# Optimization experiments

Hardware: AMD Instinct MI355X
Metric: run time of the kernel (lower is better)

## Reference

```python
import jax, jax.numpy as jnp
import numpy as np

INF = 1000000000000.0
V, H, E, B, T, S, NUM_OOV = 32000, 512, 300, 32, 32, 400, 50


def setup_inputs() -> dict:
    key = jax.random.key(0)
    ks = jax.random.split(key, 20)
    sc = 0.02
    inp = {
        'trg_seq_embedded': jax.random.normal(ks[0], (B, T, E), jnp.float32),
        'ext_src_seq': jax.random.randint(ks[1], (B, S), 0, V + NUM_OOV, jnp.int32),
        'init_states': jax.random.normal(ks[2], (1, B, H), jnp.float32),
        'encoder_outputs': jax.random.normal(ks[3], (B, S, H), jnp.float32),
        'encoder_mask': jax.random.randint(ks[4], (B, S), 0, 2, jnp.int32),
        # parameters (PyTorch Linear convention: y = x @ W.T + b)
        'W_enc': sc * jax.random.normal(ks[5], (H, H), jnp.float32),
        'b_enc': jnp.zeros((H,), jnp.float32),
        'W_red': sc * jax.random.normal(ks[6], (E, E + H), jnp.float32),
        'b_red': jnp.zeros((E,), jnp.float32),
        'W_ih': sc * jax.random.normal(ks[7], (4 * H, E), jnp.float32),
        'W_hh': sc * jax.random.normal(ks[8], (4 * H, H), jnp.float32),
        'b_ih': jnp.zeros((4 * H,), jnp.float32),
        'b_hh': jnp.zeros((4 * H,), jnp.float32),
        'W_cat': sc * jax.random.normal(ks[9], (H, 2 * H), jnp.float32),
        'b_cat': jnp.zeros((H,), jnp.float32),
        'W_log': sc * jax.random.normal(ks[10], (V, H), jnp.float32),
        'b_log': jnp.zeros((V,), jnp.float32),
    }
    return inp


def decoder_forward(trg_seq_embedded, init_states, encoder_outputs,
                    W_enc, b_enc, W_red, b_red, W_ih, W_hh, b_ih, b_hh,
                    W_cat, b_cat, W_log, b_log, ext_src_seq, encoder_mask):
    batch, max_len, _ = trg_seq_embedded.shape
    src_len = encoder_outputs.shape[1]
    hidden = encoder_outputs.shape[-1]
    memories = encoder_outputs @ W_enc.T + b_enc            # [B,S,H]
    mask0 = (encoder_mask == 0)                              # [B,S]
    bidx = jnp.arange(batch)[:, None]                        # [B,1]

    h0 = init_states[0]
    c0 = init_states[0]
    ctx0 = jnp.zeros((batch, hidden), trg_seq_embedded.dtype)
    cov0 = jnp.zeros((batch, src_len), trg_seq_embedded.dtype)

    def step(carry, emb_t):
        h, c, prev_ctx, cov = carry
        x = jnp.concatenate([emb_t, prev_ctx], axis=-1) @ W_red.T + b_red
        gates = x @ W_ih.T + b_ih + h @ W_hh.T + b_hh
        i, f, g, o = jnp.split(gates, 4, axis=-1)
        c_new = jax.nn.sigmoid(f) * c + jax.nn.sigmoid(i) * jnp.tanh(g)
        h_new = jax.nn.sigmoid(o) * jnp.tanh(c_new)
        energy = jnp.einsum('bh,bsh->bs', h_new, memories)
        energy = jnp.where(mask0, -INF, energy)
        attn = jax.nn.softmax(energy, axis=-1)
        ctx = jnp.einsum('bs,bsh->bh', attn, memories)
        logit_in = jnp.tanh(jnp.concatenate([h_new, ctx], axis=-1) @ W_cat.T + b_cat)
        logit = logit_in @ W_log.T + b_log                   # [B,V]
        ext = jnp.concatenate([logit, jnp.zeros((batch, NUM_OOV), logit.dtype)], axis=1)
        out = jnp.full_like(ext, -INF).at[bidx, ext_src_seq].max(energy)
        out = jnp.where(out == -INF, 0.0, out)
        logit_ext = ext + out
        logit_ext = jnp.where(logit_ext == 0.0, -INF, logit_ext)
        return (h_new, c_new, ctx, cov + attn), (logit_ext, attn, cov, energy)

    _, (logits, attns, covs, energies) = jax.lax.scan(
        step, (h0, c0, ctx0, cov0), jnp.swapaxes(trg_seq_embedded, 0, 1))
    return logits, attns, covs, energies


def reference(trg_seq_embedded, ext_src_seq, init_states, encoder_outputs, encoder_mask,
              W_enc, b_enc, W_red, b_red, W_ih, W_hh, b_ih, b_hh,
              W_cat, b_cat, W_log, b_log):
    return decoder_forward(trg_seq_embedded, init_states, encoder_outputs,
                           W_enc, b_enc, W_red, b_red, W_ih, W_hh, b_ih, b_hh,
                           W_cat, b_cat, W_log, b_log, ext_src_seq, encoder_mask)
```

## Files before the change

kernel.cpp:

```cpp
#include <hip/hip_runtime.h>
#include <hip/hip_bf16.h>

#define INF_F 1000000000000.0f

typedef __attribute__((ext_vector_type(8))) short bfrag8;
typedef __attribute__((ext_vector_type(4))) float facc4;
typedef __attribute__((ext_vector_type(4))) short short4v;

__device__ __forceinline__ float sigf(float x){ return 1.0f/(1.0f + expf(-x)); }
__device__ __forceinline__ short f2bf(float f){
  __hip_bfloat16 h = __float2bfloat16(f);
  return *reinterpret_cast<short*>(&h);
}
__device__ __forceinline__ float bf2f(short s){
  unsigned u = ((unsigned)(unsigned short)s) << 16;
  return *reinterpret_cast<float*>(&u);
}

#define OFF_LOG 0ull
#define OFF_A   32819200ull
#define OFF_C   33228800ull
#define OFF_E   33638400ull

__global__ __launch_bounds__(256) void k_init(const float* __restrict__ init_s,
    float* __restrict__ hbuf, float* __restrict__ c0, float* __restrict__ ctxb,
    float* __restrict__ cov) {
  int i = blockIdx.x*256 + threadIdx.x;
  if (i < 32*512) { float v = init_s[i]; hbuf[i]=v; c0[i]=v; ctxb[i]=0.0f; }
  if (i < 32*400) cov[i] = 0.0f;
}

__global__ __launch_bounds__(256) void k_bcombo(const float* __restrict__ W_ih,
    const float* __restrict__ b_red, const float* __restrict__ b_ih,
    const float* __restrict__ b_hh, float* __restrict__ bcomb) {
  int j = blockIdx.x*256 + threadIdx.x;
  if (j >= 2048) return;
  float acc = b_ih[j] + b_hh[j];
  for (int m=0;m<300;m++) acc += W_ih[j*300+m]*b_red[m];
  bcomb[j] = acc;
}

__global__ __launch_bounds__(256) void k_wcombo(const float* __restrict__ W_ih,
    const float* __restrict__ W_red, float* __restrict__ Wct) {
  __shared__ float As[16][68];
  __shared__ float Bs[16][68];
  int tid = threadIdx.x;
  int m0 = blockIdx.y*64, n0 = blockIdx.x*64;
  int rl = tid>>2, kq = (tid&3)*4;
  int kl = tid>>4, c4 = (tid&15)*4;
  int tx = tid&15, ty = tid>>4;
  float acc[4][4]={};
  for (int kk=0;kk<300;kk+=16){
    #pragma unroll
    for (int q=0;q<4;q++){
      int kg = kk+kq+q;
      As[kq+q][rl] = (kg<300) ? W_ih[(size_t)(m0+rl)*300 + kg] : 0.0f;
    }
    #pragma unroll
    for (int q=0;q<4;q++){
      int c = n0 + c4 + q;
      Bs[kl][c4+q] = (kk+kl<300 && c<812) ? W_red[(size_t)(kk+kl)*812 + c] : 0.0f;
    }
    __syncthreads();
    #pragma unroll
    for (int k=0;k<16;k++){
      const float* ap=&As[k][ty*4]; const float* bp=&Bs[k][tx*4];
      #pragma unroll
      for (int i=0;i<4;i++)
        #pragma unroll
        for (int j=0;j<4;j++) acc[i][j] += ap[i]*bp[j];
    }
    __syncthreads();
  }
  #pragma unroll
  for (int i=0;i<4;i++)
    #pragma unroll
    for (int j=0;j<4;j++){
      int row = m0+ty*4+i, col = n0+tx*4+j;
      if (col<812) Wct[(size_t)row*812 + col] = acc[i][j];
    }
}

__global__ __launch_bounds__(256) void k_gemb(const float* __restrict__ trg,
    const float* __restrict__ Wct, const float* __restrict__ bcomb,
    float* __restrict__ Gemb) {
  __shared__ float As[16][68];
  __shared__ float Bs[16][68];
  int tid = threadIdx.x;
  int m0 = blockIdx.y*64, n0 = blockIdx.x*64;
  int rl = tid>>2, kq = (tid&3)*4;
  int tx = tid&15, ty = tid>>4;
  float acc[4][4]={};
  int r = m0 + rl;
  const float* arow = trg + (size_t)(r&31)*9600 + (size_t)(r>>5)*300;
  for (int kk=0;kk<300;kk+=16){
    #pragma unroll
    for (int q=0;q<4;q++){
      int kg = kk+kq+q;
      As[kq+q][rl] = (kg<300) ? arow[kg] : 0.0f;
      Bs[kq+q][rl] = (kg<300) ? Wct[(size_t)(n0+rl)*812 + kg] : 0.0f;
    }
    __syncthreads();
    #pragma unroll
    for (int k=0;k<16;k++){
      const float* ap=&As[k][ty*4]; const float* bp=&Bs[k][tx*4];
      #pragma unroll
      for (int i=0;i<4;i++)
        #pragma unroll
        for (int j=0;j<4;j++) acc[i][j] += ap[i]*bp[j];
    }
    __syncthreads();
  }
  #pragma unroll
  for (int i=0;i<4;i++)
    #pragma unroll
    for (int j=0;j<4;j++){
      int rr = m0+ty*4+i, col = n0+tx*4+j;
      Gemb[(size_t)rr*2048 + col] = acc[i][j] + bcomb[col];
    }
}

__global__ __launch_bounds__(256) void k_wgpack(const float* __restrict__ Wct,
    const float* __restrict__ W_hh, float* __restrict__ Wg) {
  int idx = blockIdx.x*256 + threadIdx.x;
  if (idx >= 1024*2048) return;
  int k = idx >> 11, j = idx & 2047;
  Wg[idx] = (k < 512) ? Wct[(size_t)j*812 + 300 + k] : W_hh[(size_t)j*512 + (k-512)];
}

__global__ __launch_bounds__(256) void k_convsplit(const float* __restrict__ enc,
    const float* __restrict__ W_enc, short* __restrict__ ehi, short* __restrict__ elo,
    short* __restrict__ whi, short* __restrict__ wlo) {
  int i4 = blockIdx.x*256 + threadIdx.x;
  const float* src; short* dhi; short* dlo; size_t off;
  if (i4 < 1638400) { src = enc;   dhi = ehi; dlo = elo; off = (size_t)i4*4; }
  else { int j4 = i4 - 1638400; if (j4 >= 65536) return;
         src = W_enc; dhi = whi; dlo = wlo; off = (size_t)j4*4; }
  float4 v = *(const float4*)(src + off);
  float f[4] = {v.x, v.y, v.z, v.w};
  short4v h, l;
  #pragma unroll
  for (int q=0;q<4;q++){
    short hb = f2bf(f[q]);
    float r = f[q] - bf2f(hb);
    h[q] = hb; l[q] = f2bf(r);
  }
  *(short4v*)(dhi + off) = h;
  *(short4v*)(dlo + off) = l;
}

__device__ __forceinline__ int lds_off(int row, int slot) {
  return (row<<6) + (((slot ^ ((row>>1)&3))&3)<<4);
}

__global__ __launch_bounds__(256) void k_memories(const short* __restrict__ Ahg,
    const short* __restrict__ Alg, const short* __restrict__ Bhg,
    const short* __restrict__ Blg, const float* __restrict__ bias,
    float* __restrict__ mem) {
  __shared__ short Ah[4096];
  __shared__ short Al[4096];
  __shared__ short Bh[4096];
  __shared__ short Bl[4096];
  int tid = threadIdx.x;
  int m0 = blockIdx.x*128, n0 = blockIdx.y*128;
  int w = tid>>6, lane = tid&63;
  int wr = w>>1, wc = w&1;
  int lr = lane&15, kg2 = lane>>4;

  int srow = tid>>1;
  int ss   = (tid&1)*2;
  const short* gah = Ahg + (size_t)(m0+srow)*512 + ss*8;
  const short* gal = Alg + (size_t)(m0+srow)*512 + ss*8;
  const short* gbh = Bhg + (size_t)(n0+srow)*512 + ss*8;
  const short* gbl = Blg + (size_t)(n0+srow)*512 + ss*8;
  int wo0 = lds_off(srow, ss), wo1 = lds_off(srow, ss+1);

  int raoff[4], rboff[4];
  #pragma unroll
  for (int q=0;q<4;q++){
    raoff[q] = lds_off(wr*64 + q*16 + lr, kg2);
    rboff[q] = lds_off(wc*64 + q*16 + lr, kg2);
  }

  facc4 acc[4][4] = {};
  bfrag8 rah0 = *(const bfrag8*)(gah);
  bfrag8 rah1 = *(const bfrag8*)(gah+8);
  bfrag8 ral0 = *(const bfrag8*)(gal);
  bfrag8 ral1 = *(const bfrag8*)(gal+8);
  bfrag8 rbh0 = *(const bfrag8*)(gbh);
  bfrag8 rbh1 = *(const bfrag8*)(gbh+8);
  bfrag8 rbl0 = *(const bfrag8*)(gbl);
  bfrag8 rbl1 = *(const bfrag8*)(gbl+8);

  for (int i=0;i<16;i++){
    __syncthreads();
    *(bfrag8*)((char*)Ah + wo0) = rah0;
    *(bfrag8*)((char*)Ah + wo1) = rah1;
    *(bfrag8*)((char*)Al + wo0) = ral0;
    *(bfrag8*)((char*)Al + wo1) = ral1;
    *(bfrag8*)((char*)Bh + wo0) = rbh0;
    *(bfrag8*)((char*)Bh + wo1) = rbh1;
    *(bfrag8*)((char*)Bl + wo0) = rbl0;
    *(bfrag8*)((char*)Bl + wo1) = rbl1;
    __syncthreads();
    if (i<15){
      gah += 32; gal += 32; gbh += 32; gbl += 32;
      rah0 = *(const bfrag8*)(gah);
      rah1 = *(const bfrag8*)(gah+8);
      ral0 = *(const bfrag8*)(gal);
      ral1 = *(const bfrag8*)(gal+8);
      rbh0 = *(const bfrag8*)(gbh);
      rbh1 = *(const bfrag8*)(gbh+8);
      rbl0 = *(const bfrag8*)(gbl);
      rbl1 = *(const bfrag8*)(gbl+8);
    }
    bfrag8 afh[4], afl[4], bfh[4], bfl[4];
    #pragma unroll
    for (int q=0;q<4;q++){
      afh[q] = *(const bfrag8*)((char*)Ah + raoff[q]);
      afl[q] = *(const bfrag8*)((char*)Al + raoff[q]);
      bfh[q] = *(const bfrag8*)((char*)Bh + rboff[q]);
      bfl[q] = *(const bfrag8*)((char*)Bl + rboff[q]);
    }
    #pragma unroll
    for (int mi=0;mi<4;mi++)
      #pragma unroll
      for (int ni=0;ni<4;ni++){
        acc[mi][ni] = __builtin_amdgcn_mfma_f32_16x16x32_bf16(afl[mi], bfh[ni], acc[mi][ni], 0,0,0);
        acc[mi][ni] = __builtin_amdgcn_mfma_f32_16x16x32_bf16(afh[mi], bfl[ni], acc[mi][ni], 0,0,0);
        acc[mi][ni] = __builtin_amdgcn_mfma_f32_16x16x32_bf16(afh[mi], bfh[ni], acc[mi][ni], 0,0,0);
      }
  }

  #pragma unroll
  for (int mi=0;mi<4;mi++){
    int row = m0 + wr*64 + mi*16 + kg2*4;
    #pragma unroll
    for (int ni=0;ni<4;ni++){
      int col = n0 + wc*64 + ni*16 + lr;
      float bl = bias[col];
      #pragma unroll
      for (int q=0;q<4;q++)
        mem[(size_t)(row+q)*512 + col] = acc[mi][ni][q] + bl;
    }
  }
}

__global__ __launch_bounds__(256) void k_wlogconv(const float* __restrict__ W_log,
    __hip_bfloat16* __restrict__ wlb, const float* __restrict__ W_cat,
    short* __restrict__ wcatb) {
  int i4 = blockIdx.x*256 + threadIdx.x;
  if (i4 < 4096000) {
    const float4 v = *(const float4*)(W_log + (size_t)i4*4);
    size_t o = (size_t)i4*4;
    wlb[o+0] = __float2bfloat16(v.x); wlb[o+1] = __float2bfloat16(v.y);
    wlb[o+2] = __float2bfloat16(v.z); wlb[o+3] = __float2bfloat16(v.w);
  } else {
    int j4 = i4 - 4096000;
    if (j4 >= 131072) return;
    const float4 v = *(const float4*)(W_cat + (size_t)j4*4);
    short4v s;
    s[0]=f2bf(v.x); s[1]=f2bf(v.y); s[2]=f2bf(v.z); s[3]=f2bf(v.w);
    *(short4v*)(wcatb + (size_t)j4*4) = s;
  }
}

__global__ __launch_bounds__(256) void k_catconv(const float* __restrict__ hall,
    const float* __restrict__ ctxa, short* __restrict__ licat) {
  int i4 = blockIdx.x*256 + threadIdx.x;
  if (i4 >= 262144) return;
  int row = i4 >> 8, colq = (i4 & 255) * 4;
  const float* src = (colq < 512) ? (hall + (size_t)row*512 + colq)
                                  : (ctxa + (size_t)row*512 + colq - 512);
  float4 v = *(const float4*)src;
  short4v s;
  s[0]=f2bf(v.x); s[1]=f2bf(v.y); s[2]=f2bf(v.z); s[3]=f2bf(v.w);
  *(short4v*)(licat + (size_t)i4*4) = s;
}

__global__ __launch_bounds__(256) void k_gates(const float* __restrict__ ctxb,
    const float* __restrict__ hbuf, const float* __restrict__ Wg,
    float* __restrict__ partials) {
  __shared__ float yh_s[64][32];
  int ks = blockIdx.x;
  int rc = blockIdx.y;
  int tid = threadIdx.x;
  const float* side = (ks < 8) ? ctxb : hbuf;
  int kbase = (ks & 7) * 64;
  {
    int b_l = tid >> 3, kq0 = (tid & 7) * 8;
    const float* src = side + (size_t)b_l*512 + kbase + kq0;
    float4 v0 = *(const float4*)(src);
    float4 v1 = *(const float4*)(src + 4);
    yh_s[kq0+0][b_l]=v0.x; yh_s[kq0+1][b_l]=v0.y;
    yh_s[kq0+2][b_l]=v0.z; yh_s[kq0+3][b_l]=v0.w;
    yh_s[kq0+4][b_l]=v1.x; yh_s[kq0+5][b_l]=v1.y;
    yh_s[kq0+6][b_l]=v1.z; yh_s[kq0+7][b_l]=v1.w;
  }
  __syncthreads();
  int tr = tid & 31, bg = tid >> 5;
  int row0 = rc*128 + tr*4;
  float acc[4][4] = {};
  const float* wp = Wg + (size_t)(ks*64)*2048 + row0;
  #pragma unroll 8
  for (int k=0;k<64;k++){
    float4 w = *(const float4*)(wp + (size_t)k*2048);
    float4 y = *(const float4*)&yh_s[k][bg*4];
    acc[0][0]+=w.x*y.x; acc[0][1]+=w.x*y.y; acc[0][2]+=w.x*y.z; acc[0][3]+=w.x*y.w;
    acc[1][0]+=w.y*y.x; acc[1][1]+=w.y*y.y; acc[1][2]+=w.y*y.z; acc[1][3]+=w.y*y.w;
    acc[2][0]+=w.z*y.x; acc[2][1]+=w.z*y.y; acc[2][2]+=w.z*y.z; acc[2][3]+=w.z*y.w;
    acc[3][0]+=w.w*y.x; acc[3][1]+=w.w*y.y; acc[3][2]+=w.w*y.z; acc[3][3]+=w.w*y.w;
  }
  #pragma unroll
  for (int j=0;j<4;j++){
    float4 o; o.x=acc[0][j]; o.y=acc[1][j]; o.z=acc[2][j]; o.w=acc[3][j];
    *(float4*)(partials + (size_t)(ks*32 + bg*4 + j)*2048 + row0) = o;
  }
}

__global__ __launch_bounds__(256) void k_lstm_energy(const float* __restrict__ part,
    const float* __restrict__ Gemb,
    const float* __restrict__ c_in, float* __restrict__ c_out,
    float* __restrict__ hbuf, float* __restrict__ hall,
    const float* __restrict__ mem, const int* __restrict__ emask,
    float* __restrict__ out, int t) {
  __shared__ float hl[512];
  int blk = blockIdx.x, tid = threadIdx.x;
  int b = blk & 31, sc = blk >> 5;
  int r = t*32 + b;
  int lane = tid & 63, w = tid >> 6;
  const float* gp = Gemb + (size_t)r*2048;
  #pragma unroll
  for (int jj=0; jj<2; jj++){
    int j = tid + jj*256;
    float g[4];
    #pragma unroll
    for (int gi=0; gi<4; gi++){
      int row = gi*512 + j;
      float v = gp[row];
      #pragma unroll
      for (int ks=0; ks<16; ks++)
        v += part[(size_t)(ks*32+b)*2048 + row];
      g[gi] = v;
    }
    float cp = c_in[b*512+j];
    float cn = sigf(g[1])*cp + sigf(g[0])*tanhf(g[2]);
    float hn = sigf(g[3])*tanhf(cn);
    hl[j] = hn;
    if (sc==0){
      c_out[b*512+j]=cn; hbuf[b*512+j]=hn; hall[(size_t)r*512+j]=hn;
    }
  }
  __syncthreads();
  float4 h0 = *(const float4*)&hl[lane*8];
  float4 h1 = *(const float4*)&hl[lane*8+4];
  const float* mb = mem + (size_t)b*204800;
  const int* em = emask + b*400;
  for (int i=0;i<13;i++){
    int s_l = i*4 + w;
    if (s_l < 50){
      int s = sc*50 + s_l;
      const float4* mp = (const float4*)(mb + (size_t)s*512 + lane*8);
      float4 m0 = mp[0], m1 = mp[1];
      float acc = h0.x*m0.x + h0.y*m0.y + h0.z*m0.z + h0.w*m0.w
                + h1.x*m1.x + h1.y*m1.y + h1.z*m1.z + h1.w*m1.w;
      #pragma unroll
      for (int off=32; off; off>>=1) acc += __shfl_xor(acc, off);
      if (lane==0){
        out[OFF_E + (size_t)r*400 + s] = (em[s]==0) ? -INF_F : acc;
      }
    }
  }
}

__global__ __launch_bounds__(256) void k_ctx(float* __restrict__ out,
    const float* __restrict__ mem, float* __restrict__ ctxb, float* __restrict__ ctxa,
    float* __restrict__ cov, int t) {
  __shared__ float ps[400];
  __shared__ float red[8];
  __shared__ float tmp[256];
  int blk = blockIdx.x, tid = threadIdx.x;
  int b = blk & 31, hc = blk >> 5;
  int r = t*32 + b;
  int lane = tid & 63, w = tid >> 6;
  float e0 = out[OFF_E + (size_t)r*400 + tid];
  float e1 = (tid < 144) ? out[OFF_E + (size_t)r*400 + tid + 256] : -3.4e38f;
  float lm = fmaxf(e0, e1);
  #pragma unroll
  for (int off=32; off; off>>=1) lm = fmaxf(lm, __shfl_xor(lm, off));
  if (lane==0) red[w] = lm;
  __syncthreads();
  float m = fmaxf(fmaxf(red[0],red[1]), fmaxf(red[2],red[3]));
  float pv0 = expf(e0 - m);
  float pv1 = (tid < 144) ? expf(e1 - m) : 0.0f;
  float sv = pv0 + pv1;
  #pragma unroll
  for (int off=32; off; off>>=1) sv += __shfl_xor(sv, off);
  if (lane==0) red[4+w] = sv;
  __syncthreads();
  float inv = 1.0f/(red[4]+red[5]+red[6]+red[7]);
  ps[tid] = pv0*inv;
  if (tid < 144) ps[tid+256] = pv1*inv;
  __syncthreads();
  int hloc = tid & 63, sh = tid >> 6;
  int h = hc*64 + hloc;
  float acc = 0.0f;
  {
    const float* mqs = mem + (size_t)b*204800 + h + (size_t)sh*100*512;
    const float* pss = &ps[sh*100];
    #pragma unroll 10
    for (int s=0;s<100;s++) acc += pss[s]*mqs[(size_t)s*512];
  }
  tmp[sh*64 + hloc] = acc;
  __syncthreads();
  if (sh==0){
    float v = acc + tmp[64+hloc] + tmp[128+hloc] + tmp[192+hloc];
    ctxb[b*512+h] = v;
    ctxa[(size_t)r*512+h] = v;
  }
  if (hc==0){
    for (int s=tid; s<400; s+=256){
      float a = ps[s];
      out[OFF_A + (size_t)r*400 + s] = a;
      float cv = cov[b*400+s];
      out[OFF_C + (size_t)r*400 + s] = cv;
      cov[b*400+s] = cv + a;
    }
  }
}

__global__ __launch_bounds__(256) void k_logitin(const short* __restrict__ Ab,
    const short* __restrict__ Wb, const float* __restrict__ b_cat,
    __hip_bfloat16* __restrict__ lib) {
  __shared__ short As[4096];
  __shared__ short Bs[4096];
  int tid = threadIdx.x;
  int m0 = blockIdx.x*128, n0 = blockIdx.y*128;
  int w = tid>>6, lane = tid&63;
  int wr = w>>1, wc = w&1;
  int lr = lane&15, kg2 = lane>>4;

  int srow = tid>>1;
  int ss   = (tid&1)*2;
  const short* ga = Ab + (size_t)(m0+srow)*1024 + ss*8;
  const short* gw = Wb + (size_t)(n0+srow)*1024 + ss*8;
  int wo0 = lds_off(srow, ss), wo1 = lds_off(srow, ss+1);

  int raoff[4], rboff[4];
  #pragma unroll
  for (int q=0;q<4;q++){
    raoff[q] = lds_off(wr*64 + q*16 + lr, kg2);
    rboff[q] = lds_off(wc*64 + q*16 + lr, kg2);
  }

  facc4 acc[4][4] = {};
  bfrag8 ra0 = *(const bfrag8*)(ga);
  bfrag8 ra1 = *(const bfrag8*)(ga+8);
  bfrag8 rb0 = *(const bfrag8*)(gw);
  bfrag8 rb1 = *(const bfrag8*)(gw+8);

  for (int i=0;i<32;i++){
    __syncthreads();
    *(bfrag8*)((char*)As + wo0) = ra0;
    *(bfrag8*)((char*)As + wo1) = ra1;
    *(bfrag8*)((char*)Bs + wo0) = rb0;
    *(bfrag8*)((char*)Bs + wo1) = rb1;
    __syncthreads();
    if (i<31){
      ga += 32; gw += 32;
      ra0 = *(const bfrag8*)(ga);
      ra1 = *(const bfrag8*)(ga+8);
      rb0 = *(const bfrag8*)(gw);
      rb1 = *(const bfrag8*)(gw+8);
    }
    bfrag8 af[4], bf[4];
    #pragma unroll
    for (int q=0;q<4;q++){
      af[q] = *(const bfrag8*)((char*)As + raoff[q]);
      bf[q] = *(const bfrag8*)((char*)Bs + rboff[q]);
    }
    #pragma unroll
    for (int mi=0;mi<4;mi++)
      #pragma unroll
      for (int ni=0;ni<4;ni++)
        acc[mi][ni] = __builtin_amdgcn_mfma_f32_16x16x32_bf16(af[mi], bf[ni], acc[mi][ni], 0,0,0);
  }

  #pragma unroll
  for (int mi=0;mi<4;mi++){
    int row = m0 + wr*64 + mi*16 + kg2*4;
    #pragma unroll
    for (int ni=0;ni<4;ni++){
      int col = n0 + wc*64 + ni*16 + lr;
      float bc = b_cat[col];
      #pragma unroll
      for (int q=0;q<4;q++){
        float v = tanhf(acc[mi][ni][q] + bc);
        lib[(size_t)(row+q)*512 + col] = __float2bfloat16(v);
      }
    }
  }
}

__global__ __launch_bounds__(256) void k_logits(const __hip_bfloat16* __restrict__ Ab,
    const __hip_bfloat16* __restrict__ Wb, const float* __restrict__ b_log,
    float* __restrict__ out) {
  __shared__ short As[4096];
  __shared__ short Bs[4096];
  int m = blockIdx.y & 7;
  int yy = blockIdx.x + 8*(blockIdx.y >> 3);
  if (yy >= 250) return;
  int tid = threadIdx.x;
  int m0 = m*128, n0 = yy*128;
  int w = tid>>6, lane = tid&63;
  int wr = w>>1, wc = w&1;
  int lr = lane&15, kg2 = lane>>4;
  const short* A = (const short*)Ab;
  const short* W = (const short*)Wb;

  int srow = tid>>1;
  int ss   = (tid&1)*2;
  const short* ga = A + (size_t)(m0+srow)*512 + ss*8;
  const short* gw = W + (size_t)(n0+srow)*512 + ss*8;
  int wo0 = lds_off(srow, ss), wo1 = lds_off(srow, ss+1);

  int raoff[4], rboff[4];
  #pragma unroll
  for (int q=0;q<4;q++){
    raoff[q] = lds_off(wr*64 + q*16 + lr, kg2);
    rboff[q] = lds_off(wc*64 + q*16 + lr, kg2);
  }

  facc4 acc[4][4] = {};
  bfrag8 ra0 = *(const bfrag8*)(ga);
  bfrag8 ra1 = *(const bfrag8*)(ga+8);
  bfrag8 rb0 = *(const bfrag8*)(gw);
  bfrag8 rb1 = *(const bfrag8*)(gw+8);

  for (int i=0;i<16;i++){
    __syncthreads();
    *(bfrag8*)((char*)As + wo0) = ra0;
    *(bfrag8*)((char*)As + wo1) = ra1;
    *(bfrag8*)((char*)Bs + wo0) = rb0;
    *(bfrag8*)((char*)Bs + wo1) = rb1;
    __syncthreads();
    if (i<15){
      ga += 32; gw += 32;
      ra0 = *(const bfrag8*)(ga);
      ra1 = *(const bfrag8*)(ga+8);
      rb0 = *(const bfrag8*)(gw);
      rb1 = *(const bfrag8*)(gw+8);
    }
    bfrag8 af[4], bf[4];
    #pragma unroll
    for (int q=0;q<4;q++){
      af[q] = *(const bfrag8*)((char*)As + raoff[q]);
      bf[q] = *(const bfrag8*)((char*)Bs + rboff[q]);
    }
    #pragma unroll
    for (int mi=0;mi<4;mi++)
      #pragma unroll
      for (int ni=0;ni<4;ni++)
        acc[mi][ni] = __builtin_amdgcn_mfma_f32_16x16x32_bf16(af[mi], bf[ni], acc[mi][ni], 0,0,0);
  }

  #pragma unroll
  for (int mi=0;mi<4;mi++){
    int row = m0 + wr*64 + mi*16 + kg2*4;
    #pragma unroll
    for (int ni=0;ni<4;ni++){
      int col = n0 + wc*64 + ni*16 + lr;
      float bl = b_log[col];
      #pragma unroll
      for (int q=0;q<4;q++){
        float v = acc[mi][ni][q] + bl;
        out[(size_t)(row+q)*32050 + col] = (v == 0.0f) ? -INF_F : v;
      }
    }
  }
}

__global__ __launch_bounds__(512) void k_scatter(const int* __restrict__ ext_src,
    float* __restrict__ out) {
  __shared__ int tok[400];
  __shared__ float ev[400];
  int rr = blockIdx.x;
  int b = rr & 31;
  int tid = threadIdx.x;
  if (tid >= 400 && tid < 450)
    out[(size_t)rr*32050 + 32000 + (tid-400)] = -INF_F;
  if (tid < 400){
    tok[tid] = ext_src[b*400+tid];
    ev[tid]  = out[OFF_E + (size_t)rr*400 + tid];
  }
  __syncthreads();
  if (tid < 400){
    int tk = tok[tid];
    float m = -3.4e38f;
    bool pre = false;
    #pragma unroll 1
    for (int s2=0; s2<400; s2+=8){
      #pragma unroll
      for (int q=0;q<8;q++){
        int tk2 = tok[s2+q];
        float e2 = ev[s2+q];
        bool eq = (tk2==tk);
        m = fmaxf(m, eq ? e2 : -3.4e38f);
        pre = pre || (eq && (s2+q) < tid);
      }
    }
    if (!pre && m != -INF_F){
      size_t idx = (size_t)rr*32050 + tk;
      float wv = out[idx];
      float extv = (wv == -INF_F) ? 0.0f : wv;
      float nv = extv + m;
      out[idx] = (nv == 0.0f) ? -INF_F : nv;
    }
  }
}

extern "C" void kernel_launch(void* const* d_in, const int* in_sizes, int n_in,
                              void* d_out, int out_size, void* d_ws, size_t ws_size,
                              hipStream_t stream) {
  const float* trg   = (const float*)d_in[0];
  const int*   ext   = (const int*)  d_in[1];
  const float* inits = (const float*)d_in[2];
  const float* enc   = (const float*)d_in[3];
  const int*   emask = (const int*)  d_in[4];
  const float* W_enc = (const float*)d_in[5];
  const float* b_enc = (const float*)d_in[6];
  const float* W_red = (const float*)d_in[7];
  const float* b_red = (const float*)d_in[8];
  const float* W_ih  = (const float*)d_in[9];
  const float* W_hh  = (const float*)d_in[10];
  const float* b_ih  = (const float*)d_in[11];
  const float* b_hh  = (const float*)d_in[12];
  const float* W_cat = (const float*)d_in[13];
  const float* b_cat = (const float*)d_in[14];
  const float* W_log = (const float*)d_in[15];
  const float* b_log = (const float*)d_in[16];
  float* out = (float*)d_out;
  float* ws  = (float*)d_ws;

  float* mem   = ws + 0ull;
  float* Wg    = ws + 6553600ull;
  float* Wct   = ws + 8650752ull;
  float* Gemb  = ws + 10313728ull;
  float* bcomb = ws + 12410880ull;
  float* hbuf  = ws + 12412928ull;
  float* c0    = ws + 12429312ull;
  float* c1    = ws + 12445696ull;
  float* ctxb  = ws + 12462080ull;
  float* hall  = ws + 12478464ull;
  float* ctxa  = ws + 13002752ull;
  float* cov   = ws + 13527040ull;
  float* part  = ws + 13539840ull;
  __hip_bfloat16* lib = (__hip_bfloat16*)(ws + 14590464ull);
  short* licat = (short*)(ws + 8650752ull);
  short* wcatb = (short*)(ws + 9175040ull);
  __hip_bfloat16* wlb = (__hip_bfloat16*)(ws + 15245824ull);
  short* ehi = (short*)(ws + 15245824ull);
  short* elo = ehi + 6553600;
  short* whi = ehi + 13107200;
  short* wlo = ehi + 13369344;

  k_init<<<64,256,0,stream>>>(inits, hbuf, c0, ctxb, cov);
  k_bcombo<<<8,256,0,stream>>>(W_ih, b_red, b_ih, b_hh, bcomb);
  k_wcombo<<<dim3(13,32),256,0,stream>>>(W_ih, W_red, Wct);
  k_gemb<<<dim3(32,16),256,0,stream>>>(trg, Wct, bcomb, Gemb);
  k_wgpack<<<8192,256,0,stream>>>(Wct, W_hh, Wg);
  k_convsplit<<<6656,256,0,stream>>>(enc, W_enc, ehi, elo, whi, wlo);
  k_memories<<<dim3(100,4),256,0,stream>>>(ehi, elo, whi, wlo, b_enc, mem);
  k_wlogconv<<<16512,256,0,stream>>>(W_log, wlb, W_cat, wcatb);

  for (int t=0;t<32;t++){
    const float* c_in = (t&1) ? c1 : c0;
    float* c_out      = (t&1) ? c0 : c1;
    k_gates<<<dim3(16,16),256,0,stream>>>(ctxb, hbuf, Wg, part);
    k_lstm_energy<<<256,256,0,stream>>>(part, Gemb, c_in, c_out, hbuf, hall,
                                        mem, emask, out, t);
    k_ctx<<<256,256,0,stream>>>(out, mem, ctxb, ctxa, cov, t);
  }

  k_catconv<<<1024,256,0,stream>>>(hall, ctxa, licat);
  k_logitin<<<dim3(8,4),256,0,stream>>>(licat, wcatb, b_cat, lib);
  k_logits<<<dim3(8,256),256,0,stream>>>(lib, wlb, b_log, out);
  k_scatter<<<1024,512,0,stream>>>(ext, out);
}
```

Baseline: 1.178 ms.

## Widen recurrent kernels to 512 threads and write bf16 concat inputs in-loop

The per-timestep kernels k_gates, k_lstm_energy and k_ctx now launch with 512 threads per block instead of 256, so each thread does less work per step. This aims to cut latency on the serial 32-step recurrence, where grids are small. The hidden state and context are also converted to bf16 and written straight into the concatenated logit-input buffer during the loop. That removes the fp32 hall/ctxa buffers and the separate k_catconv kernel, at the cost of a few extra strided bf16 stores per step and higher per-block register and shared-memory pressure.

Result: faster. 950.0 us (-19.4%).

```diff
diff --git a/kernel.cpp b/kernel.cpp
--- a/kernel.cpp
+++ b/kernel.cpp
@@ -265,20 +265,7 @@
   }
 }
 
-__global__ __launch_bounds__(256) void k_catconv(const float* __restrict__ hall,
-    const float* __restrict__ ctxa, short* __restrict__ licat) {
-  int i4 = blockIdx.x*256 + threadIdx.x;
-  if (i4 >= 262144) return;
-  int row = i4 >> 8, colq = (i4 & 255) * 4;
-  const float* src = (colq < 512) ? (hall + (size_t)row*512 + colq)
-                                  : (ctxa + (size_t)row*512 + colq - 512);
-  float4 v = *(const float4*)src;
-  short4v s;
-  s[0]=f2bf(v.x); s[1]=f2bf(v.y); s[2]=f2bf(v.z); s[3]=f2bf(v.w);
-  *(short4v*)(licat + (size_t)i4*4) = s;
-}
-
-__global__ __launch_bounds__(256) void k_gates(const float* __restrict__ ctxb,
+__global__ __launch_bounds__(512) void k_gates(const float* __restrict__ ctxb,
     const float* __restrict__ hbuf, const float* __restrict__ Wg,
     float* __restrict__ partials) {
   __shared__ float yh_s[64][32];
@@ -288,40 +275,35 @@
   const float* side = (ks < 8) ? ctxb : hbuf;
   int kbase = (ks & 7) * 64;
   {
-    int b_l = tid >> 3, kq0 = (tid & 7) * 8;
+    int b_l = tid & 31, kq0 = (tid >> 5) * 4;
     const float* src = side + (size_t)b_l*512 + kbase + kq0;
-    float4 v0 = *(const float4*)(src);
-    float4 v1 = *(const float4*)(src + 4);
-    yh_s[kq0+0][b_l]=v0.x; yh_s[kq0+1][b_l]=v0.y;
-    yh_s[kq0+2][b_l]=v0.z; yh_s[kq0+3][b_l]=v0.w;
-    yh_s[kq0+4][b_l]=v1.x; yh_s[kq0+5][b_l]=v1.y;
-    yh_s[kq0+6][b_l]=v1.z; yh_s[kq0+7][b_l]=v1.w;
+    float4 v = *(const float4*)src;
+    yh_s[kq0+0][b_l]=v.x; yh_s[kq0+1][b_l]=v.y;
+    yh_s[kq0+2][b_l]=v.z; yh_s[kq0+3][b_l]=v.w;
   }
   __syncthreads();
-  int tr = tid & 31, bg = tid >> 5;
-  int row0 = rc*128 + tr*4;
-  float acc[4][4] = {};
+  int tr = tid & 63, bg = tid >> 6;
+  int row0 = rc*128 + tr*2;
+  float acc[2][4] = {};
   const float* wp = Wg + (size_t)(ks*64)*2048 + row0;
   #pragma unroll 8
   for (int k=0;k<64;k++){
-    float4 w = *(const float4*)(wp + (size_t)k*2048);
+    float2 w = *(const float2*)(wp + (size_t)k*2048);
     float4 y = *(const float4*)&yh_s[k][bg*4];
     acc[0][0]+=w.x*y.x; acc[0][1]+=w.x*y.y; acc[0][2]+=w.x*y.z; acc[0][3]+=w.x*y.w;
     acc[1][0]+=w.y*y.x; acc[1][1]+=w.y*y.y; acc[1][2]+=w.y*y.z; acc[1][3]+=w.y*y.w;
-    acc[2][0]+=w.z*y.x; acc[2][1]+=w.z*y.y; acc[2][2]+=w.z*y.z; acc[2][3]+=w.z*y.w;
-    acc[3][0]+=w.w*y.x; acc[3][1]+=w.w*y.y; acc[3][2]+=w.w*y.z; acc[3][3]+=w.w*y.w;
   }
   #pragma unroll
   for (int j=0;j<4;j++){
-    float4 o; o.x=acc[0][j]; o.y=acc[1][j]; o.z=acc[2][j]; o.w=acc[3][j];
-    *(float4*)(partials + (size_t)(ks*32 + bg*4 + j)*2048 + row0) = o;
-  }
-}
-
-__global__ __launch_bounds__(256) void k_lstm_energy(const float* __restrict__ part,
+    float2 o; o.x=acc[0][j]; o.y=acc[1][j];
+    *(float2*)(partials + (size_t)(ks*32 + bg*4 + j)*2048 + row0) = o;
+  }
+}
+
+__global__ __launch_bounds__(512) void k_lstm_energy(const float* __restrict__ part,
     const float* __restrict__ Gemb,
     const float* __restrict__ c_in, float* __restrict__ c_out,
-    float* __restrict__ hbuf, float* __restrict__ hall,
+    float* __restrict__ hbuf, short* __restrict__ licat,
     const float* __restrict__ mem, const int* __restrict__ emask,
     float* __restrict__ out, int t) {
   __shared__ float hl[512];
@@ -329,10 +311,9 @@
   int b = blk & 31, sc = blk >> 5;
   int r = t*32 + b;
   int lane = tid & 63, w = tid >> 6;
-  const float* gp = Gemb + (size_t)r*2048;
-  #pragma unroll
-  for (int jj=0; jj<2; jj++){
-    int j = tid + jj*256;
+  {
+    int j = tid;
+    const float* gp = Gemb + (size_t)r*2048;
     float g[4];
     #pragma unroll
     for (int gi=0; gi<4; gi++){
@@ -348,7 +329,8 @@
     float hn = sigf(g[3])*tanhf(cn);
     hl[j] = hn;
     if (sc==0){
-      c_out[b*512+j]=cn; hbuf[b*512+j]=hn; hall[(size_t)r*512+j]=hn;
+      c_out[b*512+j]=cn; hbuf[b*512+j]=hn;
+      licat[(size_t)r*1024 + j] = f2bf(hn);
     }
   }
   __syncthreads();
@@ -356,8 +338,8 @@
   float4 h1 = *(const float4*)&hl[lane*8+4];
   const float* mb = mem + (size_t)b*204800;
   const int* em = emask + b*400;
-  for (int i=0;i<13;i++){
-    int s_l = i*4 + w;
+  for (int i=0;i<7;i++){
+    int s_l = i*8 + w;
     if (s_l < 50){
       int s = sc*50 + s_l;
       const float4* mp = (const float4*)(mb + (size_t)s*512 + lane*8);
@@ -373,59 +355,61 @@
   }
 }
 
-__global__ __launch_bounds__(256) void k_ctx(float* __restrict__ out,
-    const float* __restrict__ mem, float* __restrict__ ctxb, float* __restrict__ ctxa,
+__global__ __launch_bounds__(512) void k_ctx(float* __restrict__ out,
+    const float* __restrict__ mem, float* __restrict__ ctxb, short* __restrict__ licat,
     float* __restrict__ cov, int t) {
   __shared__ float ps[400];
-  __shared__ float red[8];
-  __shared__ float tmp[256];
+  __shared__ float red[16];
+  __shared__ float tmp[512];
   int blk = blockIdx.x, tid = threadIdx.x;
   int b = blk & 31, hc = blk >> 5;
   int r = t*32 + b;
   int lane = tid & 63, w = tid >> 6;
-  float e0 = out[OFF_E + (size_t)r*400 + tid];
-  float e1 = (tid < 144) ? out[OFF_E + (size_t)r*400 + tid + 256] : -3.4e38f;
-  float lm = fmaxf(e0, e1);
+  float e = (tid < 400) ? out[OFF_E + (size_t)r*400 + tid] : -3.4e38f;
+  float lm = e;
   #pragma unroll
   for (int off=32; off; off>>=1) lm = fmaxf(lm, __shfl_xor(lm, off));
   if (lane==0) red[w] = lm;
   __syncthreads();
-  float m = fmaxf(fmaxf(red[0],red[1]), fmaxf(red[2],red[3]));
-  float pv0 = expf(e0 - m);
-  float pv1 = (tid < 144) ? expf(e1 - m) : 0.0f;
-  float sv = pv0 + pv1;
+  float m = red[0];
+  #pragma unroll
+  for (int i=1;i<8;i++) m = fmaxf(m, red[i]);
+  float pv = (tid < 400) ? expf(e - m) : 0.0f;
+  float sv = pv;
   #pragma unroll
   for (int off=32; off; off>>=1) sv += __shfl_xor(sv, off);
-  if (lane==0) red[4+w] = sv;
+  if (lane==0) red[8+w] = sv;
   __syncthreads();
-  float inv = 1.0f/(red[4]+red[5]+red[6]+red[7]);
-  ps[tid] = pv0*inv;
-  if (tid < 144) ps[tid+256] = pv1*inv;
+  float sum = red[8];
+  #pragma unroll
+  for (int i=1;i<8;i++) sum += red[8+i];
+  float inv = 1.0f/sum;
+  if (tid < 400) ps[tid] = pv*inv;
   __syncthreads();
   int hloc = tid & 63, sh = tid >> 6;
   int h = hc*64 + hloc;
   float acc = 0.0f;
   {
-    const float* mqs = mem + (size_t)b*204800 + h + (size_t)sh*100*512;
-    const float* pss = &ps[sh*100];
+    const float* mqs = mem + (size_t)b*204800 + h + (size_t)sh*50*512;
+    const float* pss = &ps[sh*50];
     #pragma unroll 10
-    for (int s=0;s<100;s++) acc += pss[s]*mqs[(size_t)s*512];
+    for (int s=0;s<50;s++) acc += pss[s]*mqs[(size_t)s*512];
   }
   tmp[sh*64 + hloc] = acc;
   __syncthreads();
   if (sh==0){
-    float v = acc + tmp[64+hloc] + tmp[128+hloc] + tmp[192+hloc];
+    float v = acc;
+    #pragma unroll
+    for (int q=1;q<8;q++) v += tmp[q*64 + hloc];
     ctxb[b*512+h] = v;
-    ctxa[(size_t)r*512+h] = v;
-  }
-  if (hc==0){
-    for (int s=tid; s<400; s+=256){
-      float a = ps[s];
-      out[OFF_A + (size_t)r*400 + s] = a;
-      float cv = cov[b*400+s];
-      out[OFF_C + (size_t)r*400 + s] = cv;
-      cov[b*400+s] = cv + a;
-    }
+    licat[(size_t)r*1024 + 512 + h] = f2bf(v);
+  }
+  if (hc==0 && tid<400){
+    float a = ps[tid];
+    out[OFF_A + (size_t)r*400 + tid] = a;
+    float cv = cov[b*400+tid];
+    out[OFF_C + (size_t)r*400 + tid] = cv;
+    cov[b*400+tid] = cv + a;
   }
 }
 
@@ -651,8 +635,6 @@
   float* c0    = ws + 12429312ull;
   float* c1    = ws + 12445696ull;
   float* ctxb  = ws + 12462080ull;
-  float* hall  = ws + 12478464ull;
-  float* ctxa  = ws + 13002752ull;
   float* cov   = ws + 13527040ull;
   float* part  = ws + 13539840ull;
   __hip_bfloat16* lib = (__hip_bfloat16*)(ws + 14590464ull);
@@ -676,13 +658,12 @@
   for (int t=0;t<32;t++){
     const float* c_in = (t&1) ? c1 : c0;
     float* c_out      = (t&1) ? c0 : c1;
-    k_gates<<<dim3(16,16),256,0,stream>>>(ctxb, hbuf, Wg, part);
-    k_lstm_energy<<<256,256,0,stream>>>(part, Gemb, c_in, c_out, hbuf, hall,
+    k_gates<<<dim3(16,16),512,0,stream>>>(ctxb, hbuf, Wg, part);
+    k_lstm_energy<<<256,512,0,stream>>>(part, Gemb, c_in, c_out, hbuf, licat,
                                         mem, emask, out, t);
-    k_ctx<<<256,256,0,stream>>>(out, mem, ctxb, ctxa, cov, t);
-  }
-
-  k_catconv<<<1024,256,0,stream>>>(hall, ctxa, licat);
+    k_ctx<<<256,512,0,stream>>>(out, mem, ctxb, licat, cov, t);
+  }
+
   k_logitin<<<dim3(8,4),256,0,stream>>>(licat, wcatb, b_cat, lib);
   k_logits<<<dim3(8,256),256,0,stream>>>(lib, wlb, b_log, out);
   k_scatter<<<1024,512,0,stream>>>(ext, out);
```
